# Kernel optimization log

Measured on AMD Instinct MI355X. Metric: run time of the kernel, lower is better.

## Reference

```python
import jax, jax.numpy as jnp
import numpy as np

DIM = 128
DEPTHS = 2
D_STATE = 16
D_CONV = 4
D_INNER = 2 * DIM          # expand=2
DT_RANK = DIM // 16        # ceil(128/16)=8


def layer_norm(x, g, b, eps=1e-5):
    mu = jnp.mean(x, axis=-1, keepdims=True)
    var = jnp.var(x, axis=-1, keepdims=True)
    return (x - mu) * jax.lax.rsqrt(var + eps) * g + b


def mamba_mixer(x, in_w, conv_w, conv_b, x_proj_w, dt_w, dt_b, A_log, Dp, out_w):
    # x: (B, L, DIM)
    Bb, L, _ = x.shape
    xz = x @ in_w                                  # (B, L, 2*D_INNER)
    xp, z = jnp.split(xz, 2, axis=-1)
    # causal depthwise conv1d over L (mamba: conv1d(padding=K-1)[..., :L])
    xpad = jnp.pad(xp, ((0, 0), (D_CONV - 1, 0), (0, 0)))
    xc = sum(xpad[:, k:k + L, :] * conv_w[:, k] for k in range(D_CONV)) + conv_b
    xc = jax.nn.silu(xc)
    x_dbl = xc @ x_proj_w                          # (B, L, DT_RANK + 2*D_STATE)
    dt = x_dbl[..., :DT_RANK]
    Bm = x_dbl[..., DT_RANK:DT_RANK + D_STATE]
    Cm = x_dbl[..., DT_RANK + D_STATE:]
    dt = jax.nn.softplus(dt @ dt_w + dt_b)         # (B, L, D_INNER)
    A = -jnp.exp(A_log)                            # (D_INNER, D_STATE)

    def step(h, inp):
        dt_t, B_t, C_t, x_t = inp                  # (B,di) (B,ds) (B,ds) (B,di)
        dA = jnp.exp(dt_t[:, :, None] * A)         # (B, di, ds)
        h = h * dA + (dt_t * x_t)[:, :, None] * B_t[:, None, :]
        y = jnp.einsum('bds,bs->bd', h, C_t)
        return h, y

    h0 = jnp.zeros((Bb, D_INNER, D_STATE), x.dtype)
    xs = (dt.transpose(1, 0, 2), Bm.transpose(1, 0, 2),
          Cm.transpose(1, 0, 2), xc.transpose(1, 0, 2))
    _, ys = jax.lax.scan(step, h0, xs)             # ys: (L, B, di)
    y = ys.transpose(1, 0, 2) + xc * Dp
    y = y * jax.nn.silu(z)
    return y @ out_w                               # (B, L, DIM)


def reference(x, skip, expand_w, pe_g, pe_b, ln_g, ln_b, in_proj_w, conv_w,
              conv_b, x_proj_w, dt_proj_w, dt_proj_b, A_log, D, out_proj_w,
              cbd_w, cbd_b):
    x = x.transpose(0, 2, 3, 1)                    # NCHW -> NHWC
    skip = skip.transpose(0, 2, 3, 1)
    # PatchExpanding: dim -> 2*dim, pixel-shuffle 2x2, LayerNorm(dim//2)
    B_, H, W, _ = x.shape
    x = x @ expand_w                               # (B, H, W, 2*DIM)
    c = x.shape[-1] // 4                           # = DIM//2
    x = x.reshape(B_, H, W, 2, 2, c).transpose(0, 1, 3, 2, 4, 5)
    x = x.reshape(B_, 2 * H, 2 * W, c)
    x = layer_norm(x, pe_g, pe_b)
    x = jnp.concatenate([x, skip], axis=-1)        # (B, 2H, 2W, DIM)
    B_, H2, W2, C = x.shape
    x = x.reshape(B_, H2 * W2, C)
    for i in range(DEPTHS):
        x = x + mamba_mixer(layer_norm(x, ln_g[i], ln_b[i]), in_proj_w[i],
                            conv_w[i], conv_b[i], x_proj_w[i], dt_proj_w[i],
                            dt_proj_b[i], A_log[i], D[i], out_proj_w[i])
    x = x @ cbd_w + cbd_b                          # (B, L, DIM//2)
    return x.reshape(B_, -1, H2, W2)               # faithful plain reshape (as torch .view)


def setup_inputs() -> dict:
    key = jax.random.key(0)
    ks = jax.random.split(key, 10)
    B, H, W = 2, 48, 48
    s = 0.02
    f32 = jnp.float32
    dt_init = float(np.log(np.expm1(0.01)))
    return {
        'x': jax.random.normal(ks[0], (B, DIM, H, W), f32),
        'skip': jax.random.normal(ks[1], (B, DIM // 2, 2 * H, 2 * W), f32),
        'expand_w': (jax.random.normal(ks[2], (DIM, 2 * DIM), f32) * s),
        'pe_g': jnp.ones((DIM // 2,), f32),
        'pe_b': jnp.zeros((DIM // 2,), f32),
        'ln_g': jnp.ones((DEPTHS, DIM), f32),
        'ln_b': jnp.zeros((DEPTHS, DIM), f32),
        'in_proj_w': jax.random.normal(ks[3], (DEPTHS, DIM, 2 * D_INNER), f32) * s,
        'conv_w': jax.random.normal(ks[4], (DEPTHS, D_INNER, D_CONV), f32) * 0.1,
        'conv_b': jnp.zeros((DEPTHS, D_INNER), f32),
        'x_proj_w': jax.random.normal(ks[5], (DEPTHS, D_INNER, DT_RANK + 2 * D_STATE), f32) * s,
        'dt_proj_w': jax.random.normal(ks[6], (DEPTHS, DT_RANK, D_INNER), f32) * 0.1,
        'dt_proj_b': jnp.full((DEPTHS, D_INNER), dt_init, f32),
        'A_log': jnp.log(jnp.broadcast_to(jnp.arange(1, D_STATE + 1, dtype=f32), (DEPTHS, D_INNER, D_STATE))),
        'D': jnp.ones((DEPTHS, D_INNER), f32),
        'out_proj_w': jax.random.normal(ks[7], (DEPTHS, D_INNER, DIM), f32) * s,
        'cbd_w': jax.random.normal(ks[8], (DIM, DIM // 2), f32) * s,
        'cbd_b': jnp.zeros((DIM // 2,), f32),
    }
```

## Files before the change

### kernel.cpp

```cpp
#include <hip/hip_runtime.h>
#include <hip/hip_bf16.h>

#define LB   9216
#define NB   2
#define ROWS (NB*LB)
#define NCH  576
#define CHL  16
#define NGRP 32
#define GSZ  18

#define YST 264
#define LST 136

typedef __hip_bfloat16  bf16;
typedef __hip_bfloat162 bf162;
typedef __attribute__((ext_vector_type(8))) short short8;
typedef __attribute__((ext_vector_type(4))) float f32x4;
typedef __attribute__((ext_vector_type(2))) float f32x2;

__device__ __forceinline__ float silu_f(float v) { return v / (1.f + __expf(-v)); }
__device__ __forceinline__ float softplus_f(float v) {
    return fmaxf(v, 0.f) + log1pf(__expf(-fabsf(v)));
}
__device__ __forceinline__ float ldm(const void* p, int j, bool bfm) {
    return bfm ? __bfloat162float(((const bf16*)p)[j]) : ((const float*)p)[j];
}
__device__ __forceinline__ short8 pack_bf8(const float* v) {
    union { short8 s; bf16 b[8]; } u;
    #pragma unroll
    for (int i = 0; i < 8; ++i) u.b[i] = __float2bfloat16(v[i]);
    return u.s;
}
__device__ __forceinline__ void build_pw2(float e1, f32x2* pw2) {
    float e2 = e1 * e1;
    f32x2 M2 = (f32x2){e2, e2};
    f32x2 M4 = M2 * M2;
    f32x2 M8 = M4 * M4;
    pw2[0] = (f32x2){e1, e2};
    pw2[1] = pw2[0] * M2;
    pw2[2] = pw2[0] * M4;
    pw2[3] = pw2[1] * M4;
    pw2[4] = pw2[0] * M8;
    pw2[5] = pw2[1] * M8;
    pw2[6] = pw2[2] * M8;
    pw2[7] = pw2[3] * M8;
}
__device__ __forceinline__ bool load_astruct2(const float* Atab, int dep, int d,
                                              float& A0, f32x2* cs2) {
    const f32x4* Ap = (const f32x4*)(Atab + dep * 4096 + d * 16);
    float A[16];
    #pragma unroll
    for (int i = 0; i < 4; ++i) {
        f32x4 v = Ap[i];
        A[4*i] = v[0]; A[4*i+1] = v[1]; A[4*i+2] = v[2]; A[4*i+3] = v[3];
    }
    A0 = A[0];
    bool structured = true;
    #pragma unroll
    for (int s = 0; s < 16; ++s) {
        float c = A[s] - (float)(s + 1) * A0;
        structured = structured &&
            (fabsf(c) <= 0.03f * (float)(s + 1) * fabsf(A0) + 1e-6f);
        cs2[s >> 1][s & 1] = c;
    }
    return structured;
}

struct CvtArgs { const void* src[18]; int off[19]; };
#define PREP_CVT   274624
#define PREP_IPWT  131072
#define PREP_OPWT  65536
#define PREP_XPWT  24576
#define PREP_CBWT  8192
#define PREP_ATAB  8192
#define PREP_TOTAL (PREP_CVT + PREP_IPWT + PREP_OPWT + PREP_XPWT + PREP_CBWT + PREP_ATAB)
__global__ void k_prep(CvtArgs a, float* __restrict__ dst,
                       bf16* __restrict__ ipwT, bf16* __restrict__ opwT,
                       bf16* __restrict__ xpwT48, bf16* __restrict__ cbwT,
                       float* __restrict__ Atab) {
    int i = blockIdx.x * 256 + threadIdx.x;
    if (i >= PREP_TOTAL) return;
    bool bfm = (*(const unsigned int*)a.src[13]) != 0u;
    if (i < PREP_CVT) {
        int s = 0;
        while (i >= a.off[s + 1]) ++s;
        dst[i] = ldm(a.src[s], i - a.off[s], bfm);
    } else if (i < PREP_CVT + PREP_IPWT) {
        int j = i - PREP_CVT;
        int dep = j >> 16, r = j & 65535;
        int n = r >> 7, k = r & 127;
        ipwT[j] = __float2bfloat16(ldm(a.src[7], dep * 65536 + k * 512 + n, bfm));
    } else if (i < PREP_CVT + PREP_IPWT + PREP_OPWT) {
        int j = i - PREP_CVT - PREP_IPWT;
        int dep = j >> 15, r = j & 32767;
        int n = r >> 8, k = r & 255;
        opwT[j] = __float2bfloat16(ldm(a.src[15], dep * 32768 + k * 128 + n, bfm));
    } else if (i < PREP_CVT + PREP_IPWT + PREP_OPWT + PREP_XPWT) {
        int j = i - PREP_CVT - PREP_IPWT - PREP_OPWT;
        int dep = j / 12288, r = j % 12288;
        int o = r >> 8, k = r & 255;
        xpwT48[j] = (o < 40) ? __float2bfloat16(ldm(a.src[10], dep * 10240 + k * 40 + o, bfm))
                             : __float2bfloat16(0.f);
    } else if (i < PREP_CVT + PREP_IPWT + PREP_OPWT + PREP_XPWT + PREP_CBWT) {
        int j = i - PREP_CVT - PREP_IPWT - PREP_OPWT - PREP_XPWT;
        int n = j >> 7, k = j & 127;
        cbwT[j] = __float2bfloat16(ldm(a.src[16], k * 64 + n, bfm));
    } else {
        int j = i - PREP_CVT - PREP_IPWT - PREP_OPWT - PREP_XPWT - PREP_CBWT;
        Atab[j] = -__expf(ldm(a.src[13], j, bfm));
    }
}

__global__ void k_expand(const void* __restrict__ xraw, const void* __restrict__ skipraw,
                         const float* __restrict__ ew, const float* __restrict__ peg,
                         const float* __restrict__ peb, float* __restrict__ x0,
                         const void* __restrict__ alog_raw) {
    bool bfm = (*(const unsigned int*)alog_raw) != 0u;
    int blk = blockIdx.x;
    int b = blk / 2304;
    int rem = blk - b * 2304;
    int h = rem / 48, w = rem - h * 48;
    int t = threadIdx.x;
    __shared__ float xv[128];
    if (t < 128) xv[t] = ldm(xraw, b * 294912 + t * 2304 + h * 48 + w, bfm);
    __syncthreads();
    float acc = 0.f;
    #pragma unroll 8
    for (int k = 0; k < 128; ++k)
        acc += xv[k] * ew[k * 256 + t];
    int q = t >> 6, c = t & 63;
    int h2 = 2 * h + (q >> 1), w2 = 2 * w + (q & 1);
    int row = b * LB + h2 * 96 + w2;
    float s = acc, sq = acc * acc;
    #pragma unroll
    for (int m = 32; m >= 1; m >>= 1) {
        s  += __shfl_xor(s, m);
        sq += __shfl_xor(sq, m);
    }
    float mu  = s * (1.f / 64.f);
    float var = sq * (1.f / 64.f) - mu * mu;
    float rs  = rsqrtf(var + 1e-5f);
    x0[row * 128 + c]      = (acc - mu) * rs * peg[c] + peb[c];
    x0[row * 128 + 64 + c] = ldm(skipraw, b * 589824 + c * 9216 + h2 * 96 + w2, bfm);
}

__global__ void k_lngemm_in(const float* __restrict__ x0, const float* __restrict__ g,
                            const float* __restrict__ bb, const bf16* __restrict__ ipwT,
                            bf16* __restrict__ xz, int dep) {
    __shared__ bf16 lnt[16 * LST];
    int row0 = blockIdx.x * 16;
    int t = threadIdx.x;
    int w = t >> 6, lane = t & 63;
    for (int r = w; r < 16; r += 4) {
        float v0 = x0[(size_t)(row0 + r) * 128 + lane];
        float v1 = x0[(size_t)(row0 + r) * 128 + 64 + lane];
        float s = v0 + v1, sq = v0 * v0 + v1 * v1;
        #pragma unroll
        for (int m = 32; m >= 1; m >>= 1) { s += __shfl_xor(s, m); sq += __shfl_xor(sq, m); }
        float mu  = s * (1.f / 128.f);
        float var = sq * (1.f / 128.f) - mu * mu;
        float rs  = rsqrtf(var + 1e-5f);
        lnt[r * LST + lane]      = __float2bfloat16((v0 - mu) * rs * g[dep * 128 + lane]      + bb[dep * 128 + lane]);
        lnt[r * LST + 64 + lane] = __float2bfloat16((v1 - mu) * rs * g[dep * 128 + 64 + lane] + bb[dep * 128 + 64 + lane]);
    }
    __syncthreads();
    int m = lane & 15, quad = lane >> 4;
    short8 av[4];
    #pragma unroll
    for (int ks = 0; ks < 4; ++ks)
        av[ks] = *(const short8*)&lnt[m * LST + ks * 32 + quad * 8];
    const bf16* wb = ipwT + (size_t)dep * 65536;
    #pragma unroll
    for (int j = 0; j < 8; ++j) {
        int nt = w * 8 + j;
        f32x4 acc = (f32x4){0.f, 0.f, 0.f, 0.f};
        #pragma unroll
        for (int ks = 0; ks < 4; ++ks) {
            short8 bv = *(const short8*)&wb[(nt * 16 + m) * 128 + ks * 32 + quad * 8];
            acc = __builtin_amdgcn_mfma_f32_16x16x32_bf16(av[ks], bv, acc, 0, 0, 0);
        }
        #pragma unroll
        for (int reg = 0; reg < 4; ++reg)
            xz[(size_t)(row0 + quad * 4 + reg) * 512 + nt * 16 + m] = __float2bfloat16(acc[reg]);
    }
}

__global__ void k_convxp(const bf16* __restrict__ xz, const float* __restrict__ cw,
                         const float* __restrict__ cb, const bf16* __restrict__ xpwT48,
                         const float* __restrict__ dtw, const float* __restrict__ dtb,
                         bf16* __restrict__ xc, bf16* __restrict__ dt,
                         bf16* __restrict__ Bm, bf16* __restrict__ Cm, int dep) {
    __shared__ bf16 xsb[16 * YST];
    __shared__ float xdbl[16 * 48];
    int row0 = blockIdx.x * 16;
    int l0 = row0 % LB;
    int t = threadIdx.x;
    {
        float xw[19];
        #pragma unroll
        for (int r = 0; r < 19; ++r) {
            int gr = row0 - 3 + r;
            bool valid = !(l0 == 0 && r < 3);
            xw[r] = valid ? __bfloat162float(xz[(size_t)gr * 512 + t]) : 0.f;
        }
        float cwv[4];
        #pragma unroll
        for (int k = 0; k < 4; ++k) cwv[k] = cw[dep * 1024 + t * 4 + k];
        float cb0 = cb[dep * 256 + t];
        #pragma unroll
        for (int i = 0; i < 16; ++i) {
            float s = cb0;
            #pragma unroll
            for (int k = 0; k < 4; ++k) s += xw[i + k] * cwv[k];
            s = silu_f(s);
            bf16 sb = __float2bfloat16(s);
            xsb[i * YST + t] = sb;
            xc[(size_t)(row0 + i) * 256 + t] = sb;
        }
    }
    __syncthreads();
    int wv = t >> 6, lane = t & 63;
    int m = lane & 15, quad = lane >> 4;
    if (wv < 3) {
        const bf16* wb = xpwT48 + (size_t)dep * 12288 + (size_t)(wv * 16 + m) * 256;
        const bf16* arow = &xsb[m * YST];
        f32x4 acc = (f32x4){0.f, 0.f, 0.f, 0.f};
        #pragma unroll
        for (int ks = 0; ks < 8; ++ks) {
            short8 av = *(const short8*)&arow[ks * 32 + quad * 8];
            short8 bv = *(const short8*)&wb[ks * 32 + quad * 8];
            acc = __builtin_amdgcn_mfma_f32_16x16x32_bf16(av, bv, acc, 0, 0, 0);
        }
        #pragma unroll
        for (int reg = 0; reg < 4; ++reg)
            xdbl[(quad * 4 + reg) * 48 + wv * 16 + m] = acc[reg];
    }
    __syncthreads();
    {
        float wj[8];
        #pragma unroll
        for (int j = 0; j < 8; ++j) wj[j] = dtw[dep * 2048 + j * 256 + t];
        float b0 = dtb[dep * 256 + t];
        #pragma unroll
        for (int r = 0; r < 16; ++r) {
            float a = b0;
            #pragma unroll
            for (int j = 0; j < 8; ++j) a += xdbl[r * 48 + j] * wj[j];
            dt[(size_t)(row0 + r) * 256 + t] = __float2bfloat16(softplus_f(a));
        }
    }
    {
        int r = t >> 4, s = t & 15;
        Bm[(size_t)(row0 + r) * 16 + s] = __float2bfloat16(xdbl[r * 48 + 8 + s]);
        Cm[(size_t)(row0 + r) * 16 + s] = __float2bfloat16(xdbl[r * 48 + 24 + s]);
    }
}

__global__ void k_scan1(const bf16* __restrict__ dt, const bf16* __restrict__ xc,
                        const bf16* __restrict__ Bm, const float* __restrict__ Atab,
                        bf16* __restrict__ hend, bf16* __restrict__ aprod,
                        int dep, int nch, int chl) {
    __shared__ __align__(16) char smem1[1024 + 8192 + 8192];
    float* Bs  = (float*)smem1;
    bf16*  dts = (bf16*)(smem1 + 1024);
    bf16*  xcs = (bf16*)(smem1 + 1024 + 8192);
    int blk = blockIdx.x;
    int b = blk / nch, ch = blk - b * nch;
    int d = threadIdx.x;
    int rb = b * LB + ch * chl;
    {
        const short8* g1 = (const short8*)(dt + (size_t)rb * 256);
        const short8* g2 = (const short8*)(xc + (size_t)rb * 256);
        short8* s1 = (short8*)dts;
        short8* s2 = (short8*)xcs;
        s1[d] = g1[d]; s1[d + 256] = g1[d + 256];
        s2[d] = g2[d]; s2[d + 256] = g2[d + 256];
    }
    {
        int r = d >> 4, c = d & 15;
        Bs[d] = __bfloat162float(Bm[(size_t)(rb + r) * 16 + c]);
    }
    __syncthreads();
    float A0;
    f32x2 cs2[8], h2[8];
    bool structured = load_astruct2(Atab, dep, d, A0, cs2);
    #pragma unroll
    for (int i = 0; i < 8; ++i) h2[i] = (f32x2){0.f, 0.f};
    float sdt = 0.f;
    if (structured) {
        for (int t = 0; t < chl; ++t) {
            float dtv = __bfloat162float(dts[t * 256 + d]);
            float xv  = __bfloat162float(xcs[t * 256 + d]);
            sdt += dtv;
            float dtx = dtv * xv;
            f32x2 pw2[8];
            build_pw2(__expf(dtv * A0), pw2);
            f32x2 dtv2 = (f32x2){dtv, dtv}, dtx2 = (f32x2){dtx, dtx};
            const f32x2* Bp2 = (const f32x2*)&Bs[t * 16];
            #pragma unroll
            for (int i = 0; i < 8; ++i) {
                f32x2 a = pw2[i] * (dtv2 * cs2[i]) + pw2[i];
                h2[i] = h2[i] * a + dtx2 * Bp2[i];
            }
        }
    } else {
        for (int t = 0; t < chl; ++t) {
            float dtv = __bfloat162float(dts[t * 256 + d]);
            float xv  = __bfloat162float(xcs[t * 256 + d]);
            sdt += dtv;
            float dtx = dtv * xv;
            #pragma unroll
            for (int s = 0; s < 16; ++s) {
                float As = fmaf((float)(s + 1), A0, cs2[s >> 1][s & 1]);
                float a = __expf(dtv * As);
                h2[s >> 1][s & 1] = fmaf(h2[s >> 1][s & 1], a, dtx * Bs[t * 16 + s]);
            }
        }
    }
    size_t base = (size_t)blk * 4096 + (size_t)d * 16;
    float hv[16], apv[16];
    #pragma unroll
    for (int i = 0; i < 8; ++i) { hv[2*i] = h2[i][0]; hv[2*i+1] = h2[i][1]; }
    if (structured) {
        f32x2 pw2[8];
        build_pw2(__expf(sdt * A0), pw2);
        f32x2 sdt2 = (f32x2){sdt, sdt};
        #pragma unroll
        for (int i = 0; i < 8; ++i) {
            f32x2 ap = pw2[i] * (sdt2 * cs2[i]) + pw2[i];
            apv[2*i] = ap[0]; apv[2*i+1] = ap[1];
        }
    } else {
        #pragma unroll
        for (int s = 0; s < 16; ++s) {
            float As = fmaf((float)(s + 1), A0, cs2[s >> 1][s & 1]);
            apv[s] = __expf(sdt * As);
        }
    }
    *(short8*)(hend + base)      = pack_bf8(hv);
    *(short8*)(hend + base + 8)  = pack_bf8(hv + 8);
    *(short8*)(aprod + base)     = pack_bf8(apv);
    *(short8*)(aprod + base + 8) = pack_bf8(apv + 8);
}

__global__ void k_scan2a(const bf16* __restrict__ hend, const bf16* __restrict__ aprod,
                         float* __restrict__ gA, float* __restrict__ gH, int nch) {
    int g = blockIdx.x >> 5;
    int p = (blockIdx.x & 31) * 256 + threadIdx.x;
    int b = p >> 12, rem = p & 4095;
    int ch0 = g * GSZ;
    size_t base = (size_t)(b * nch + ch0) * 4096 + rem;
    float ap[GSZ], he[GSZ];
    #pragma unroll
    for (int j = 0; j < GSZ; ++j) {
        ap[j] = __bfloat162float(aprod[base + (size_t)j * 4096]);
        he[j] = __bfloat162float(hend[base + (size_t)j * 4096]);
    }
    float ga = 1.f, gh = 0.f;
    #pragma unroll
    for (int j = 0; j < GSZ; ++j) {
        gh = fmaf(gh, ap[j], he[j]);
        ga *= ap[j];
    }
    gA[g * 8192 + p] = ga;
    gH[g * 8192 + p] = gh;
}

__global__ void k_scan2bc(bf16* __restrict__ hend, const bf16* __restrict__ aprod,
                          const float* __restrict__ gA, const float* __restrict__ gH,
                          int nch) {
    int g = blockIdx.x >> 5;
    int p = (blockIdx.x & 31) * 256 + threadIdx.x;
    int b = p >> 12, rem = p & 4095;
    float h = 0.f;
    for (int gg = 0; gg < g; ++gg)
        h = fmaf(h, gA[gg * 8192 + p], gH[gg * 8192 + p]);
    int ch0 = g * GSZ;
    size_t base = (size_t)(b * nch + ch0) * 4096 + rem;
    float ap[GSZ], he[GSZ];
    #pragma unroll
    for (int j = 0; j < GSZ; ++j) {
        ap[j] = __bfloat162float(aprod[base + (size_t)j * 4096]);
        he[j] = __bfloat162float(hend[base + (size_t)j * 4096]);
    }
    #pragma unroll
    for (int j = 0; j < GSZ; ++j) {
        hend[base + (size_t)j * 4096] = __float2bfloat16(h);
        h = fmaf(h, ap[j], he[j]);
    }
}

__device__ __forceinline__ void scan3_core(const bf16* dts, const bf16* xcs,
                                           const bf16* zs, const float* Atab,
                                           const float* Dp, const bf16* hstart,
                                           int dep, int blk, int d,
                                           const float* Bs, const float* Cs,
                                           bf16* ybuf) {
    size_t base = (size_t)blk * 4096 + (size_t)d * 16;
    float A0;
    f32x2 cs2[8], h2[8];
    bool structured = load_astruct2(Atab, dep, d, A0, cs2);
    {
        union { short8 s; bf16 b[8]; } u0, u1;
        u0.s = *(const short8*)(hstart + base);
        u1.s = *(const short8*)(hstart + base + 8);
        #pragma unroll
        for (int i = 0; i < 4; ++i) {
            h2[i]     = (f32x2){__bfloat162float(u0.b[2*i]), __bfloat162float(u0.b[2*i+1])};
            h2[4 + i] = (f32x2){__bfloat162float(u1.b[2*i]), __bfloat162float(u1.b[2*i+1])};
        }
    }
    float Dv = Dp[dep * 256 + d];
    if (structured) {
        #pragma unroll
        for (int r = 0; r < CHL; ++r) {
            float dtv = __bfloat162float(dts[r * 256 + d]);
            float xv  = __bfloat162float(xcs[r * 256 + d]);
            float zv  = __bfloat162float(zs[r * 256 + d]);
            float dtx = dtv * xv;
            f32x2 pw2[8];
            build_pw2(__expf(dtv * A0), pw2);
            f32x2 dtv2 = (f32x2){dtv, dtv}, dtx2 = (f32x2){dtx, dtx};
            f32x2 y2 = (f32x2){0.f, 0.f};
            const f32x2* Bp2 = (const f32x2*)&Bs[r * 16];
            const f32x2* Cp2 = (const f32x2*)&Cs[r * 16];
            #pragma unroll
            for (int i = 0; i < 8; ++i) {
                f32x2 a = pw2[i] * (dtv2 * cs2[i]) + pw2[i];
                h2[i] = h2[i] * a + dtx2 * Bp2[i];
                y2 = h2[i] * Cp2[i] + y2;
            }
            float y = y2[0] + y2[1];
            y = (y + xv * Dv) * silu_f(zv);
            ybuf[r * YST + d] = __float2bfloat16(y);
        }
    } else {
        #pragma unroll
        for (int r = 0; r < CHL; ++r) {
            float dtv = __bfloat162float(dts[r * 256 + d]);
            float xv  = __bfloat162float(xcs[r * 256 + d]);
            float zv  = __bfloat162float(zs[r * 256 + d]);
            float dtx = dtv * xv;
            float y = 0.f;
            #pragma unroll
            for (int s = 0; s < 16; ++s) {
                float As = fmaf((float)(s + 1), A0, cs2[s >> 1][s & 1]);
                float a = __expf(dtv * As);
                float hv = fmaf(h2[s >> 1][s & 1], a, dtx * Bs[r * 16 + s]);
                h2[s >> 1][s & 1] = hv;
                y = fmaf(hv, Cs[r * 16 + s], y);
            }
            y = (y + xv * Dv) * silu_f(zv);
            ybuf[r * YST + d] = __float2bfloat16(y);
        }
    }
}

__device__ __forceinline__ void stage_scan3(const bf16* dt, const bf16* xc,
                                            const bf16* xz, int row0, int t,
                                            bf16* dts, bf16* xcs, bf16* zs) {
    const short8* g1 = (const short8*)(dt + (size_t)row0 * 256);
    const short8* g2 = (const short8*)(xc + (size_t)row0 * 256);
    short8* s1 = (short8*)dts;
    short8* s2 = (short8*)xcs;
    s1[t] = g1[t]; s1[t + 256] = g1[t + 256];
    s2[t] = g2[t]; s2[t + 256] = g2[t + 256];
    #pragma unroll
    for (int k = 0; k < 2; ++k) {
        int v = t + k * 256;
        int r = v >> 5, d8 = v & 31;
        ((short8*)zs)[v] = *(const short8*)&xz[(size_t)(row0 + r) * 512 + 256 + d8 * 8];
    }
}

__global__ __launch_bounds__(256, 4)
void k_scan3_out0(const bf16* __restrict__ dt, const bf16* __restrict__ xc,
                  const bf16* __restrict__ Bm, const bf16* __restrict__ Cm,
                  bf16* __restrict__ xz, const float* __restrict__ Atab,
                  const float* __restrict__ Dp, const bf16* __restrict__ hstart,
                  float* __restrict__ x0, const float* __restrict__ g,
                  const float* __restrict__ bb, const bf16* __restrict__ ipwT,
                  const bf16* __restrict__ opwT) {
    __shared__ __align__(16) char smem[2048 + 16 * YST * 2 + 24576];
    float* Bs  = (float*)smem;
    float* Cs  = (float*)(smem + 1024);
    bf16*  ybuf= (bf16*)(smem + 2048);
    char*  stg = smem + 2048 + 16 * YST * 2;
    bf16*  dts = (bf16*)stg;
    bf16*  xcs = (bf16*)(stg + 8192);
    bf16*  zs  = (bf16*)(stg + 16384);
    float* x0s = (float*)stg;
    bf16*  lnt = (bf16*)(stg + 8448);
    int blk = blockIdx.x;
    int row0 = blk * 16;
    int t = threadIdx.x;
    f32x4 rx0[2];
    {
        const f32x4* gx = (const f32x4*)(x0 + (size_t)row0 * 128);
        rx0[0] = gx[t]; rx0[1] = gx[t + 256];
    }
    stage_scan3(dt, xc, xz, row0, t, dts, xcs, zs);
    {
        int r = t >> 4, c = t & 15;
        Bs[t] = __bfloat162float(Bm[(size_t)(row0 + r) * 16 + c]);
        Cs[t] = __bfloat162float(Cm[(size_t)(row0 + r) * 16 + c]);
    }
    __syncthreads();
    scan3_core(dts, xcs, zs, Atab, Dp, hstart, 0, blk, t, Bs, Cs, ybuf);
    __syncthreads();
    #pragma unroll
    for (int k = 0; k < 2; ++k) {
        int v = t + k * 256;
        int r = v >> 5, c4 = v & 31;
        *(f32x4*)&x0s[r * 132 + c4 * 4] = rx0[k];
    }
    __syncthreads();
    int w = t >> 6, lane = t & 63;
    int m = lane & 15, quad = lane >> 4;
    {
        short8 av[8];
        #pragma unroll
        for (int ks = 0; ks < 8; ++ks)
            av[ks] = *(const short8*)&ybuf[m * YST + ks * 32 + quad * 8];
        #pragma unroll
        for (int j = 0; j < 2; ++j) {
            int nt = w * 2 + j;
            f32x4 acc = (f32x4){0.f, 0.f, 0.f, 0.f};
            #pragma unroll
            for (int ks = 0; ks < 8; ++ks) {
                short8 bv = *(const short8*)&opwT[(nt * 16 + m) * 256 + ks * 32 + quad * 8];
                acc = __builtin_amdgcn_mfma_f32_16x16x32_bf16(av[ks], bv, acc, 0, 0, 0);
            }
            #pragma unroll
            for (int reg = 0; reg < 4; ++reg)
                x0s[(quad * 4 + reg) * 132 + nt * 16 + m] += acc[reg];
        }
    }
    __syncthreads();
    for (int r = w; r < 16; r += 4) {
        float v0 = x0s[r * 132 + lane], v1 = x0s[r * 132 + 64 + lane];
        float s = v0 + v1, sq = v0 * v0 + v1 * v1;
        #pragma unroll
        for (int mm = 32; mm >= 1; mm >>= 1) { s += __shfl_xor(s, mm); sq += __shfl_xor(sq, mm); }
        float mu  = s * (1.f / 128.f);
        float var = sq * (1.f / 128.f) - mu * mu;
        float rs  = rsqrtf(var + 1e-5f);
        lnt[r * LST + lane]      = __float2bfloat16((v0 - mu) * rs * g[128 + lane] + bb[128 + lane]);
        lnt[r * LST + 64 + lane] = __float2bfloat16((v1 - mu) * rs * g[192 + lane] + bb[192 + lane]);
    }
    #pragma unroll
    for (int k = 0; k < 2; ++k) {
        int v = t + k * 256;
        int r = v >> 5, c4 = v & 31;
        ((f32x4*)(x0 + (size_t)row0 * 128))[v] = *(const f32x4*)&x0s[r * 132 + c4 * 4];
    }
    __syncthreads();
    {
        short8 av2[4];
        #pragma unroll
        for (int ks = 0; ks < 4; ++ks)
            av2[ks] = *(const short8*)&lnt[m * LST + ks * 32 + quad * 8];
        const bf16* wb = ipwT + 65536;
        #pragma unroll
        for (int j = 0; j < 8; ++j) {
            int nt = w * 8 + j;
            f32x4 acc = (f32x4){0.f, 0.f, 0.f, 0.f};
            #pragma unroll
            for (int ks = 0; ks < 4; ++ks) {
                short8 bv = *(const short8*)&wb[(nt * 16 + m) * 128 + ks * 32 + quad * 8];
                acc = __builtin_amdgcn_mfma_f32_16x16x32_bf16(av2[ks], bv, acc, 0, 0, 0);
            }
            #pragma unroll
            for (int reg = 0; reg < 4; ++reg)
                xz[(size_t)(row0 + quad * 4 + reg) * 512 + nt * 16 + m] = __float2bfloat16(acc[reg]);
        }
    }
}

__global__ __launch_bounds__(256, 4)
void k_scan3_out1(const bf16* __restrict__ dt, const bf16* __restrict__ xc,
                  const bf16* __restrict__ Bm, const bf16* __restrict__ Cm,
                  bf16* __restrict__ xz, const float* __restrict__ Atab,
                  const float* __restrict__ Dp, const bf16* __restrict__ hstart,
                  const float* __restrict__ x0, const bf16* __restrict__ opwT,
                  const bf16* __restrict__ cbwT, const float* __restrict__ cbb,
                  void* __restrict__ out, const void* __restrict__ alog_raw) {
    __shared__ __align__(16) char smem[2048 + 16 * YST * 2 + 24576];
    float* Bs  = (float*)smem;
    float* Cs  = (float*)(smem + 1024);
    bf16*  ybuf= (bf16*)(smem + 2048);
    char*  stg = smem + 2048 + 16 * YST * 2;
    bf16*  dts = (bf16*)stg;
    bf16*  xcs = (bf16*)(stg + 8192);
    bf16*  zs  = (bf16*)(stg + 16384);
    float* x0s = (float*)stg;
    bf16*  xfs = (bf16*)(stg + 8448);
    int blk = blockIdx.x;
    int row0 = blk * 16;
    int t = threadIdx.x;
    f32x4 rx0[2];
    {
        const f32x4* gx = (const f32x4*)(x0 + (size_t)row0 * 128);
        rx0[0] = gx[t]; rx0[1] = gx[t + 256];
    }
    stage_scan3(dt, xc, xz, row0, t, dts, xcs, zs);
    {
        int r = t >> 4, c = t & 15;
        Bs[t] = __bfloat162float(Bm[(size_t)(row0 + r) * 16 + c]);
        Cs[t] = __bfloat162float(Cm[(size_t)(row0 + r) * 16 + c]);
    }
    __syncthreads();
    scan3_core(dts, xcs, zs, Atab, Dp, hstart, 1, blk, t, Bs, Cs, ybuf);
    __syncthreads();
    #pragma unroll
    for (int k = 0; k < 2; ++k) {
        int v = t + k * 256;
        int r = v >> 5, c4 = v & 31;
        *(f32x4*)&x0s[r * 132 + c4 * 4] = rx0[k];
    }
    __syncthreads();
    int w = t >> 6, lane = t & 63;
    int m = lane & 15, quad = lane >> 4;
    {
        short8 av[8];
        #pragma unroll
        for (int ks = 0; ks < 8; ++ks)
            av[ks] = *(const short8*)&ybuf[m * YST + ks * 32 + quad * 8];
        const bf16* wb = opwT + 32768;
        #pragma unroll
        for (int j = 0; j < 2; ++j) {
            int nt = w * 2 + j;
            f32x4 acc = (f32x4){0.f, 0.f, 0.f, 0.f};
            #pragma unroll
            for (int ks = 0; ks < 8; ++ks) {
                short8 bv = *(const short8*)&wb[(nt * 16 + m) * 256 + ks * 32 + quad * 8];
                acc = __builtin_amdgcn_mfma_f32_16x16x32_bf16(av[ks], bv, acc, 0, 0, 0);
            }
            #pragma unroll
            for (int reg = 0; reg < 4; ++reg) {
                int lr  = quad * 4 + reg;
                int col = nt * 16 + m;
                xfs[lr * LST + col] = __float2bfloat16(x0s[lr * 132 + col] + acc[reg]);
            }
        }
    }
    __syncthreads();
    {
        short8 av2[4];
        #pragma unroll
        for (int ks = 0; ks < 4; ++ks)
            av2[ks] = *(const short8*)&xfs[m * LST + ks * 32 + quad * 8];
        bool bfm = (*(const unsigned int*)alog_raw) != 0u;
        int nt = w;
        f32x4 acc = (f32x4){0.f, 0.f, 0.f, 0.f};
        #pragma unroll
        for (int ks = 0; ks < 4; ++ks) {
            short8 bv = *(const short8*)&cbwT[(nt * 16 + m) * 128 + ks * 32 + quad * 8];
            acc = __builtin_amdgcn_mfma_f32_16x16x32_bf16(av2[ks], bv, acc, 0, 0, 0);
        }
        #pragma unroll
        for (int reg = 0; reg < 4; ++reg) {
            int grow = row0 + quad * 4 + reg;
            int col  = nt * 16 + m;
            float v = acc[reg] + cbb[col];
            int idx = grow * 64 + col;
            if (bfm) ((bf16*)out)[idx] = __float2bfloat16(v);
            else     ((float*)out)[idx] = v;
        }
    }
}

extern "C" void kernel_launch(void* const* d_in, const int* in_sizes, int n_in,
                              void* d_out, int out_size, void* d_ws, size_t ws_size,
                              hipStream_t stream) {
    (void)in_sizes; (void)n_in; (void)out_size; (void)ws_size;
    static const int sz[18] = {0, 0, 32768, 64, 64, 256, 256, 131072,
                               2048, 512, 20480, 4096, 512, 8192, 512, 65536, 8192, 64};
    CvtArgs ca;
    int off = 0;
    for (int i = 0; i < 18; ++i) { ca.src[i] = d_in[i]; ca.off[i] = off; off += sz[i]; }
    ca.off[18] = off;

    float* wf     = (float*)d_ws;
    bf16*  ipwT   = (bf16*)(wf + PREP_CVT);
    bf16*  opwT   = ipwT + PREP_IPWT;
    bf16*  xpwT48 = opwT + PREP_OPWT;
    bf16*  cbwT   = xpwT48 + PREP_XPWT;
    float* Atab   = (float*)(cbwT + PREP_CBWT);
    float* x0     = Atab + PREP_ATAB;
    bf16*  xz     = (bf16*)(x0 + (size_t)ROWS * 128);
    bf16*  xc     = xz + (size_t)ROWS * 512;
    bf16*  dt     = xc + (size_t)ROWS * 256;
    bf16*  Bm     = dt + (size_t)ROWS * 256;
    bf16*  Cm     = Bm + (size_t)ROWS * 16;
    bf16*  hend   = Cm + (size_t)ROWS * 16;
    bf16*  aprod  = hend + (size_t)NB * NCH * 4096;
    float* gA     = (float*)(aprod + (size_t)NB * NCH * 4096);
    float* gH     = gA + NGRP * 8192;

    const float* ew   = wf + ca.off[2];
    const float* peg  = wf + ca.off[3];
    const float* peb  = wf + ca.off[4];
    const float* lng  = wf + ca.off[5];
    const float* lnb  = wf + ca.off[6];
    const float* cw   = wf + ca.off[8];
    const float* cb   = wf + ca.off[9];
    const float* dtw  = wf + ca.off[11];
    const float* dtb  = wf + ca.off[12];
    const float* Dp   = wf + ca.off[14];
    const float* cbb  = wf + ca.off[17];

    k_prep   <<<(PREP_TOTAL + 255) / 256, 256, 0, stream>>>(ca, wf, ipwT, opwT, xpwT48, cbwT, Atab);
    k_expand <<<NB * 48 * 48, 256, 0, stream>>>(d_in[0], d_in[1], ew, peg, peb, x0, d_in[13]);
    k_lngemm_in<<<ROWS / 16, 256, 0, stream>>>(x0, lng, lnb, ipwT, xz, 0);
    for (int dep = 0; dep < 2; ++dep) {
        k_convxp <<<ROWS / 16, 256, 0, stream>>>(xz, cw, cb, xpwT48, dtw, dtb, xc, dt, Bm, Cm, dep);
        k_scan1  <<<NB * NCH, 256, 0, stream>>>(dt, xc, Bm, Atab, hend, aprod, dep, NCH, CHL);
        k_scan2a <<<NGRP * 32, 256, 0, stream>>>(hend, aprod, gA, gH, NCH);
        k_scan2bc<<<NGRP * 32, 256, 0, stream>>>(hend, aprod, gA, gH, NCH);
        if (dep == 0)
            k_scan3_out0<<<ROWS / 16, 256, 0, stream>>>(dt, xc, Bm, Cm, xz, Atab, Dp, hend,
                                                        x0, lng, lnb, ipwT, opwT);
        else
            k_scan3_out1<<<ROWS / 16, 256, 0, stream>>>(dt, xc, Bm, Cm, xz, Atab, Dp, hend,
                                                        x0, opwT, cbwT, cbb, d_out, d_in[13]);
    }
}
```

Measured before the change: 330.2 us.

## Fuse chunk-local scan pass into conv/x_proj kernel and preload scan start states

Merges the first chunked-scan pass into the conv + x_proj + dt kernel. Since both use 16-row tiles that line up with the 16-step chunks, the scan reads dt, xc and B straight from shared memory instead of reloading them from global memory in a separate launch. The scan3 kernels also load the per-chunk start state into registers at kernel entry instead of inside the core, so that load can overlap with staging. The cost is more shared memory and a longer serial tail per conv block, which may lower occupancy.

```diff
diff --git a/kernel.cpp b/kernel.cpp
--- a/kernel.cpp
+++ b/kernel.cpp
@@ -189,10 +189,15 @@
                          const float* __restrict__ cb, const bf16* __restrict__ xpwT48,
                          const float* __restrict__ dtw, const float* __restrict__ dtb,
                          bf16* __restrict__ xc, bf16* __restrict__ dt,
-                         bf16* __restrict__ Bm, bf16* __restrict__ Cm, int dep) {
-    __shared__ bf16 xsb[16 * YST];
+                         bf16* __restrict__ Bm, bf16* __restrict__ Cm,
+                         const float* __restrict__ Atab, bf16* __restrict__ hend,
+                         bf16* __restrict__ aprod, int dep) {
+    __shared__ bf16  xsb[16 * YST];
     __shared__ float xdbl[16 * 48];
-    int row0 = blockIdx.x * 16;
+    __shared__ bf16  dts[16 * 256];
+    __shared__ float Bsf[256];
+    int blk = blockIdx.x;
+    int row0 = blk * 16;
     int l0 = row0 % LB;
     int t = threadIdx.x;
     {
@@ -219,21 +224,23 @@
         }
     }
     __syncthreads();
-    int wv = t >> 6, lane = t & 63;
-    int m = lane & 15, quad = lane >> 4;
-    if (wv < 3) {
-        const bf16* wb = xpwT48 + (size_t)dep * 12288 + (size_t)(wv * 16 + m) * 256;
-        const bf16* arow = &xsb[m * YST];
-        f32x4 acc = (f32x4){0.f, 0.f, 0.f, 0.f};
-        #pragma unroll
-        for (int ks = 0; ks < 8; ++ks) {
-            short8 av = *(const short8*)&arow[ks * 32 + quad * 8];
-            short8 bv = *(const short8*)&wb[ks * 32 + quad * 8];
-            acc = __builtin_amdgcn_mfma_f32_16x16x32_bf16(av, bv, acc, 0, 0, 0);
-        }
-        #pragma unroll
-        for (int reg = 0; reg < 4; ++reg)
-            xdbl[(quad * 4 + reg) * 48 + wv * 16 + m] = acc[reg];
+    {
+        int wv = t >> 6, lane = t & 63;
+        int m = lane & 15, quad = lane >> 4;
+        if (wv < 3) {
+            const bf16* wb = xpwT48 + (size_t)dep * 12288 + (size_t)(wv * 16 + m) * 256;
+            const bf16* arow = &xsb[m * YST];
+            f32x4 acc = (f32x4){0.f, 0.f, 0.f, 0.f};
+            #pragma unroll
+            for (int ks = 0; ks < 8; ++ks) {
+                short8 av = *(const short8*)&arow[ks * 32 + quad * 8];
+                short8 bv = *(const short8*)&wb[ks * 32 + quad * 8];
+                acc = __builtin_amdgcn_mfma_f32_16x16x32_bf16(av, bv, acc, 0, 0, 0);
+            }
+            #pragma unroll
+            for (int reg = 0; reg < 4; ++reg)
+                xdbl[(quad * 4 + reg) * 48 + wv * 16 + m] = acc[reg];
+        }
     }
     __syncthreads();
     {
@@ -246,101 +253,82 @@
             float a = b0;
             #pragma unroll
             for (int j = 0; j < 8; ++j) a += xdbl[r * 48 + j] * wj[j];
-            dt[(size_t)(row0 + r) * 256 + t] = __float2bfloat16(softplus_f(a));
+            bf16 dv = __float2bfloat16(softplus_f(a));
+            dt[(size_t)(row0 + r) * 256 + t] = dv;
+            dts[r * 256 + t] = dv;
         }
     }
     {
         int r = t >> 4, s = t & 15;
-        Bm[(size_t)(row0 + r) * 16 + s] = __float2bfloat16(xdbl[r * 48 + 8 + s]);
+        bf16 bv = __float2bfloat16(xdbl[r * 48 + 8 + s]);
+        Bm[(size_t)(row0 + r) * 16 + s] = bv;
         Cm[(size_t)(row0 + r) * 16 + s] = __float2bfloat16(xdbl[r * 48 + 24 + s]);
-    }
-}
-
-__global__ void k_scan1(const bf16* __restrict__ dt, const bf16* __restrict__ xc,
-                        const bf16* __restrict__ Bm, const float* __restrict__ Atab,
-                        bf16* __restrict__ hend, bf16* __restrict__ aprod,
-                        int dep, int nch, int chl) {
-    __shared__ __align__(16) char smem1[1024 + 8192 + 8192];
-    float* Bs  = (float*)smem1;
-    bf16*  dts = (bf16*)(smem1 + 1024);
-    bf16*  xcs = (bf16*)(smem1 + 1024 + 8192);
-    int blk = blockIdx.x;
-    int b = blk / nch, ch = blk - b * nch;
-    int d = threadIdx.x;
-    int rb = b * LB + ch * chl;
-    {
-        const short8* g1 = (const short8*)(dt + (size_t)rb * 256);
-        const short8* g2 = (const short8*)(xc + (size_t)rb * 256);
-        short8* s1 = (short8*)dts;
-        short8* s2 = (short8*)xcs;
-        s1[d] = g1[d]; s1[d + 256] = g1[d + 256];
-        s2[d] = g2[d]; s2[d + 256] = g2[d + 256];
-    }
-    {
-        int r = d >> 4, c = d & 15;
-        Bs[d] = __bfloat162float(Bm[(size_t)(rb + r) * 16 + c]);
-    }
-    __syncthreads();
-    float A0;
-    f32x2 cs2[8], h2[8];
-    bool structured = load_astruct2(Atab, dep, d, A0, cs2);
-    #pragma unroll
-    for (int i = 0; i < 8; ++i) h2[i] = (f32x2){0.f, 0.f};
-    float sdt = 0.f;
-    if (structured) {
-        for (int t = 0; t < chl; ++t) {
-            float dtv = __bfloat162float(dts[t * 256 + d]);
-            float xv  = __bfloat162float(xcs[t * 256 + d]);
-            sdt += dtv;
-            float dtx = dtv * xv;
+        Bsf[t] = __bfloat162float(bv);
+    }
+    __syncthreads();
+    {
+        int d = t;
+        float A0;
+        f32x2 cs2[8], h2[8];
+        bool structured = load_astruct2(Atab, dep, d, A0, cs2);
+        #pragma unroll
+        for (int i = 0; i < 8; ++i) h2[i] = (f32x2){0.f, 0.f};
+        float sdt = 0.f;
+        if (structured) {
+            for (int ts = 0; ts < CHL; ++ts) {
+                float dtv = __bfloat162float(dts[ts * 256 + d]);
+                float xv  = __bfloat162float(xsb[ts * YST + d]);
+                sdt += dtv;
+                float dtx = dtv * xv;
+                f32x2 pw2[8];
+                build_pw2(__expf(dtv * A0), pw2);
+                f32x2 dtv2 = (f32x2){dtv, dtv}, dtx2 = (f32x2){dtx, dtx};
+                const f32x2* Bp2 = (const f32x2*)&Bsf[ts * 16];
+                #pragma unroll
+                for (int i = 0; i < 8; ++i) {
+                    f32x2 a = pw2[i] * (dtv2 * cs2[i]) + pw2[i];
+                    h2[i] = h2[i] * a + dtx2 * Bp2[i];
+                }
+            }
+        } else {
+            for (int ts = 0; ts < CHL; ++ts) {
+                float dtv = __bfloat162float(dts[ts * 256 + d]);
+                float xv  = __bfloat162float(xsb[ts * YST + d]);
+                sdt += dtv;
+                float dtx = dtv * xv;
+                #pragma unroll
+                for (int s = 0; s < 16; ++s) {
+                    float As = fmaf((float)(s + 1), A0, cs2[s >> 1][s & 1]);
+                    float a = __expf(dtv * As);
+                    h2[s >> 1][s & 1] = fmaf(h2[s >> 1][s & 1], a, dtx * Bsf[ts * 16 + s]);
+                }
+            }
+        }
+        size_t base = (size_t)blk * 4096 + (size_t)d * 16;
+        float hv[16], apv[16];
+        #pragma unroll
+        for (int i = 0; i < 8; ++i) { hv[2*i] = h2[i][0]; hv[2*i+1] = h2[i][1]; }
+        if (structured) {
             f32x2 pw2[8];
-            build_pw2(__expf(dtv * A0), pw2);
-            f32x2 dtv2 = (f32x2){dtv, dtv}, dtx2 = (f32x2){dtx, dtx};
-            const f32x2* Bp2 = (const f32x2*)&Bs[t * 16];
+            build_pw2(__expf(sdt * A0), pw2);
+            f32x2 sdt2 = (f32x2){sdt, sdt};
             #pragma unroll
             for (int i = 0; i < 8; ++i) {
-                f32x2 a = pw2[i] * (dtv2 * cs2[i]) + pw2[i];
-                h2[i] = h2[i] * a + dtx2 * Bp2[i];
-            }
-        }
-    } else {
-        for (int t = 0; t < chl; ++t) {
-            float dtv = __bfloat162float(dts[t * 256 + d]);
-            float xv  = __bfloat162float(xcs[t * 256 + d]);
-            sdt += dtv;
-            float dtx = dtv * xv;
+                f32x2 ap = pw2[i] * (sdt2 * cs2[i]) + pw2[i];
+                apv[2*i] = ap[0]; apv[2*i+1] = ap[1];
+            }
+        } else {
             #pragma unroll
             for (int s = 0; s < 16; ++s) {
                 float As = fmaf((float)(s + 1), A0, cs2[s >> 1][s & 1]);
-                float a = __expf(dtv * As);
-                h2[s >> 1][s & 1] = fmaf(h2[s >> 1][s & 1], a, dtx * Bs[t * 16 + s]);
-            }
-        }
-    }
-    size_t base = (size_t)blk * 4096 + (size_t)d * 16;
-    float hv[16], apv[16];
-    #pragma unroll
-    for (int i = 0; i < 8; ++i) { hv[2*i] = h2[i][0]; hv[2*i+1] = h2[i][1]; }
-    if (structured) {
-        f32x2 pw2[8];
-        build_pw2(__expf(sdt * A0), pw2);
-        f32x2 sdt2 = (f32x2){sdt, sdt};
-        #pragma unroll
-        for (int i = 0; i < 8; ++i) {
-            f32x2 ap = pw2[i] * (sdt2 * cs2[i]) + pw2[i];
-            apv[2*i] = ap[0]; apv[2*i+1] = ap[1];
-        }
-    } else {
-        #pragma unroll
-        for (int s = 0; s < 16; ++s) {
-            float As = fmaf((float)(s + 1), A0, cs2[s >> 1][s & 1]);
-            apv[s] = __expf(sdt * As);
-        }
-    }
-    *(short8*)(hend + base)      = pack_bf8(hv);
-    *(short8*)(hend + base + 8)  = pack_bf8(hv + 8);
-    *(short8*)(aprod + base)     = pack_bf8(apv);
-    *(short8*)(aprod + base + 8) = pack_bf8(apv + 8);
+                apv[s] = __expf(sdt * As);
+            }
+        }
+        *(short8*)(hend + base)      = pack_bf8(hv);
+        *(short8*)(hend + base + 8)  = pack_bf8(hv + 8);
+        *(short8*)(aprod + base)     = pack_bf8(apv);
+        *(short8*)(aprod + base + 8) = pack_bf8(apv + 8);
+    }
 }
 
 __global__ void k_scan2a(const bf16* __restrict__ hend, const bf16* __restrict__ aprod,
@@ -392,18 +380,17 @@
 
 __device__ __forceinline__ void scan3_core(const bf16* dts, const bf16* xcs,
                                            const bf16* zs, const float* Atab,
-                                           const float* Dp, const bf16* hstart,
-                                           int dep, int blk, int d,
+                                           const float* Dp,
+                                           short8 h0s, short8 h1s,
+                                           int dep, int d,
                                            const float* Bs, const float* Cs,
                                            bf16* ybuf) {
-    size_t base = (size_t)blk * 4096 + (size_t)d * 16;
     float A0;
     f32x2 cs2[8], h2[8];
     bool structured = load_astruct2(Atab, dep, d, A0, cs2);
     {
         union { short8 s; bf16 b[8]; } u0, u1;
-        u0.s = *(const short8*)(hstart + base);
-        u1.s = *(const short8*)(hstart + base + 8);
+        u0.s = h0s; u1.s = h1s;
         #pragma unroll
         for (int i = 0; i < 4; ++i) {
             h2[i]     = (f32x2){__bfloat162float(u0.b[2*i]), __bfloat162float(u0.b[2*i+1])};
@@ -495,9 +482,13 @@
     int row0 = blk * 16;
     int t = threadIdx.x;
     f32x4 rx0[2];
+    short8 h0s, h1s;
     {
         const f32x4* gx = (const f32x4*)(x0 + (size_t)row0 * 128);
         rx0[0] = gx[t]; rx0[1] = gx[t + 256];
+        size_t hbase = (size_t)blk * 4096 + (size_t)t * 16;
+        h0s = *(const short8*)(hstart + hbase);
+        h1s = *(const short8*)(hstart + hbase + 8);
     }
     stage_scan3(dt, xc, xz, row0, t, dts, xcs, zs);
     {
@@ -506,7 +497,7 @@
         Cs[t] = __bfloat162float(Cm[(size_t)(row0 + r) * 16 + c]);
     }
     __syncthreads();
-    scan3_core(dts, xcs, zs, Atab, Dp, hstart, 0, blk, t, Bs, Cs, ybuf);
+    scan3_core(dts, xcs, zs, Atab, Dp, h0s, h1s, 0, t, Bs, Cs, ybuf);
     __syncthreads();
     #pragma unroll
     for (int k = 0; k < 2; ++k) {
@@ -599,9 +590,13 @@
     int row0 = blk * 16;
     int t = threadIdx.x;
     f32x4 rx0[2];
+    short8 h0s, h1s;
     {
         const f32x4* gx = (const f32x4*)(x0 + (size_t)row0 * 128);
         rx0[0] = gx[t]; rx0[1] = gx[t + 256];
+        size_t hbase = (size_t)blk * 4096 + (size_t)t * 16;
+        h0s = *(const short8*)(hstart + hbase);
+        h1s = *(const short8*)(hstart + hbase + 8);
     }
     stage_scan3(dt, xc, xz, row0, t, dts, xcs, zs);
     {
@@ -610,7 +605,7 @@
         Cs[t] = __bfloat162float(Cm[(size_t)(row0 + r) * 16 + c]);
     }
     __syncthreads();
-    scan3_core(dts, xcs, zs, Atab, Dp, hstart, 1, blk, t, Bs, Cs, ybuf);
+    scan3_core(dts, xcs, zs, Atab, Dp, h0s, h1s, 1, t, Bs, Cs, ybuf);
     __syncthreads();
     #pragma unroll
     for (int k = 0; k < 2; ++k) {
@@ -714,8 +709,8 @@
     k_expand <<<NB * 48 * 48, 256, 0, stream>>>(d_in[0], d_in[1], ew, peg, peb, x0, d_in[13]);
     k_lngemm_in<<<ROWS / 16, 256, 0, stream>>>(x0, lng, lnb, ipwT, xz, 0);
     for (int dep = 0; dep < 2; ++dep) {
-        k_convxp <<<ROWS / 16, 256, 0, stream>>>(xz, cw, cb, xpwT48, dtw, dtb, xc, dt, Bm, Cm, dep);
-        k_scan1  <<<NB * NCH, 256, 0, stream>>>(dt, xc, Bm, Atab, hend, aprod, dep, NCH, CHL);
+        k_convxp <<<ROWS / 16, 256, 0, stream>>>(xz, cw, cb, xpwT48, dtw, dtb, xc, dt, Bm, Cm,
+                                                 Atab, hend, aprod, dep);
         k_scan2a <<<NGRP * 32, 256, 0, stream>>>(hend, aprod, gA, gH, NCH);
         k_scan2bc<<<NGRP * 32, 256, 0, stream>>>(hend, aprod, gA, gH, NCH);
         if (dep == 0)
```

After: 316.0 us. -4.3%, faster.
